# Kernel tuning notes

Measured on AMD Instinct MI355X. Metric: run time of the kernel, lower is better.

Reference implementation:

```python
import jax, jax.numpy as jnp
import numpy as np

B, C, N, K = 8, 192, 3136, 9
COUT = 384


def setup_inputs() -> dict:
    key = jax.random.key(0)
    k1, k2, k3, k4 = jax.random.split(key, 4)
    x = jax.random.normal(k1, (B, C, N, 1), dtype=jnp.float32)
    edge_index = jax.random.randint(k2, (2, B, N, K), 0, N, dtype=jnp.int64)
    # 1x1 conv params: BasicConv([2C, COUT]) with bias, act='relu'
    W = jax.random.normal(k3, (COUT, 2 * C), dtype=jnp.float32) * (1.0 / np.sqrt(2 * C))
    b = jax.random.normal(k4, (COUT,), dtype=jnp.float32) * 0.01
    return {"x": x, "edge_index": edge_index, "W": W, "b": b}


def _gather(xs, idx):
    # xs: [B, C, N]; idx: [B, N, K] -> [B, C, N, K]
    return jax.vmap(lambda xb, ib: xb[:, ib])(xs, idx)


def reference(x, edge_index, W, b):
    xs = x[..., 0]                       # [B, C, N]
    x_i = _gather(xs, edge_index[1])     # [B, C, N, K] center features
    x_j = _gather(xs, edge_index[0])     # [B, C, N, K] neighbor features
    feat = jnp.concatenate([x_i, x_j - x_i], axis=1)  # [B, 2C, N, K]
    # 1x1 conv + bias + relu
    h = jnp.einsum('oi,bink->bonk', W, feat) + b[None, :, None, None]
    h = jax.nn.relu(h)                   # [B, COUT, N, K]
    return jnp.max(h, axis=-1, keepdims=True)  # [B, COUT, N, 1]
```

## Files before the change

kernel.cpp:

```cpp
#include <hip/hip_runtime.h>
#include <hip/hip_bf16.h>


#define Bb   8
#define Cc   192
#define Nn   3136
#define Kk   9
#define CO   384
#define TWOC 384
#define JTOT 768
#define PADC 200

typedef short  short8 __attribute__((ext_vector_type(8)));
typedef float  f32x4  __attribute__((ext_vector_type(4)));

__device__ __forceinline__ float bf2f(unsigned int u16) {
    union { unsigned int i; float f; } c;
    c.i = u16 << 16;
    return c.f;
}
__device__ __forceinline__ short f2bf(float f) {
    __hip_bfloat16 h = __float2bfloat16(f);
    short s; __builtin_memcpy(&s, &h, 2); return s;
}

__global__ __launch_bounds__(64) void detect(const unsigned short* __restrict__ xu,
                                             const int* __restrict__ ei,
                                             int* __restrict__ flags) {
    const int lane = threadIdx.x;
    unsigned int u = xu[2 * lane];
    int bige = (((u >> 7) & 0xFFu) >= 0x88u);
    unsigned long long bf = __ballot(bige);
    int oddnz = (ei[2 * lane + 1] != 0);
    unsigned long long bo = __ballot(oddnz);
    if (lane == 0) {
        flags[0] = (bf != 0ull) ? 1 : 0;
        flags[1] = (bo == 0ull) ? 1 : 0;
    }
}

__global__ __launch_bounds__(256) void prep_AT(const void* __restrict__ W_,
                                               short* __restrict__ A_Tb,
                                               const int* __restrict__ flags) {
    const int fp32 = flags[0];
    int t = blockIdx.x * 256 + threadIdx.x;
    if (t >= JTOT * Cc) return;
    int j = t / Cc;
    int c = t - j * Cc;
    int row = (j < CO) ? j : (j - CO);
    float w1, w2;
    if (fp32) {
        const float* W = (const float*)W_;
        w1 = W[row * TWOC + c];  w2 = W[row * TWOC + Cc + c];
    } else {
        const unsigned short* W = (const unsigned short*)W_;
        w1 = bf2f(W[row * TWOC + c]);  w2 = bf2f(W[row * TWOC + Cc + c]);
    }
    A_Tb[(size_t)j * PADC + c] = f2bf((j < CO) ? (w1 - w2) : w2);
}

__global__ __launch_bounds__(256) void transpose_x(const void* __restrict__ x_,
                                                   short* __restrict__ xT,
                                                   const int* __restrict__ flags) {
    __shared__ float s[64][33];
    const int fp32 = flags[0];
    const int n0 = blockIdx.x * 64;
    const int c0 = blockIdx.y * 32;
    const int b  = blockIdx.z;
    const int t  = threadIdx.x;
    const int cl   = t >> 3;
    const int nseg = t & 7;

    if (fp32) {
        const float* p = (const float*)x_ + ((size_t)b * Cc + c0 + cl) * Nn + n0 + nseg * 8;
        float4 v0 = *(const float4*)p;
        float4 v1 = *(const float4*)(p + 4);
        int nb = nseg * 8;
        s[nb + 0][cl] = v0.x;  s[nb + 1][cl] = v0.y;
        s[nb + 2][cl] = v0.z;  s[nb + 3][cl] = v0.w;
        s[nb + 4][cl] = v1.x;  s[nb + 5][cl] = v1.y;
        s[nb + 6][cl] = v1.z;  s[nb + 7][cl] = v1.w;
    } else {
        const unsigned short* p = (const unsigned short*)x_ + ((size_t)b * Cc + c0 + cl) * Nn + n0 + nseg * 8;
        ushort4 u0 = *(const ushort4*)p;
        ushort4 u1 = *(const ushort4*)(p + 4);
        int nb = nseg * 8;
        s[nb + 0][cl] = bf2f(u0.x);  s[nb + 1][cl] = bf2f(u0.y);
        s[nb + 2][cl] = bf2f(u0.z);  s[nb + 3][cl] = bf2f(u0.w);
        s[nb + 4][cl] = bf2f(u1.x);  s[nb + 5][cl] = bf2f(u1.y);
        s[nb + 6][cl] = bf2f(u1.z);  s[nb + 7][cl] = bf2f(u1.w);
    }
    __syncthreads();

    const int nl = t >> 2;
    const int cs = t & 3;
    short8 o;
#pragma unroll
    for (int i = 0; i < 8; ++i) o[i] = f2bf(s[nl][cs * 8 + i]);
    *(short8*)(xT + ((size_t)b * Nn + n0 + nl) * PADC + c0 + cs * 8) = o;
}

#define MT 64
#define NT 256
#define KT 32
#define LPAD 40

__global__ __launch_bounds__(256) void gemm_mfma(const short* __restrict__ xT,
                                                 const short* __restrict__ A_Tb,
                                                 short* __restrict__ U,
                                                 short* __restrict__ V) {
    __shared__ short Asl[MT * LPAD];
    __shared__ short Bsl[NT * LPAD];

    const int n0 = blockIdx.x * MT;
    const int j0 = blockIdx.y * NT;
    const int b  = blockIdx.z;
    const int tid  = threadIdx.x;
    const int w    = tid >> 6;
    const int lane = tid & 63;
    const int col  = lane & 15;
    const int quad = lane >> 4;

    f32x4 acc[4][4];
#pragma unroll
    for (int i = 0; i < 4; ++i)
#pragma unroll
        for (int jf = 0; jf < 4; ++jf) acc[i][jf] = (f32x4)(0.0f);

    const int ar = tid >> 2;
    const int ag = tid & 3;

    for (int c0 = 0; c0 < Cc; c0 += KT) {
        *(short8*)(Asl + ar * LPAD + ag * 8) =
            *(const short8*)(xT + ((size_t)b * Nn + n0 + ar) * PADC + c0 + ag * 8);
#pragma unroll
        for (int h = 0; h < 4; ++h) {
            int row = h * 64 + ar;
            *(short8*)(Bsl + row * LPAD + ag * 8) =
                *(const short8*)(A_Tb + (size_t)(j0 + row) * PADC + c0 + ag * 8);
        }
        __syncthreads();

        short8 bf[4];
#pragma unroll
        for (int jf = 0; jf < 4; ++jf)
            bf[jf] = *(const short8*)(&Bsl[(w * 64 + jf * 16 + col) * LPAD + quad * 8]);
#pragma unroll
        for (int fm = 0; fm < 4; ++fm) {
            short8 a = *(const short8*)(&Asl[(fm * 16 + col) * LPAD + quad * 8]);
#pragma unroll
            for (int jf = 0; jf < 4; ++jf)
                acc[fm][jf] = __builtin_amdgcn_mfma_f32_16x16x32_bf16(a, bf[jf], acc[fm][jf], 0, 0, 0);
        }
        __syncthreads();
    }

    const int jbase = j0 + w * 64;
#pragma unroll
    for (int fn = 0; fn < 4; ++fn) {
        int j = jbase + fn * 16 + col;
        short* dst; int jj;
        if (j < CO) { dst = U; jj = j; } else { dst = V; jj = j - CO; }
#pragma unroll
        for (int fm = 0; fm < 4; ++fm) {
#pragma unroll
            for (int r = 0; r < 4; ++r) {
                int n = n0 + fm * 16 + quad * 4 + r;
                dst[((size_t)(b * Nn + n)) * CO + jj] = f2bf(acc[fm][fn][r]);
            }
        }
    }
}

__global__ __launch_bounds__(384) void gather_max(const int* __restrict__ ei,
                                                  const short* __restrict__ U,
                                                  const short* __restrict__ V,
                                                  const void* __restrict__ bias_,
                                                  void* __restrict__ out_,
                                                  const int* __restrict__ flags) {
    __shared__ float sm[32][193];
    __shared__ int si0[32][Kk];
    __shared__ int si1[32][Kk];

    const int fp32 = flags[0];
    const int is64 = flags[1];
    const int bid  = blockIdx.x;
    const int b    = bid & 7;
    const int rest = bid >> 3;
    const int half = rest / 98;
    const int n0   = (rest % 98) * 32;
    const int tid  = threadIdx.x;

    for (int s = tid; s < 32 * 2 * Kk; s += 384) {
        int ln = s / (2 * Kk);
        int slot = s - ln * (2 * Kk);
        int n = n0 + ln;
        size_t pos; int* dstp;
        if (slot < Kk) { pos = ((size_t)b * Nn + n) * Kk + slot;               dstp = &si0[ln][slot]; }
        else           { pos = ((size_t)(Bb + b) * Nn + n) * Kk + (slot - Kk); dstp = &si1[ln][slot - Kk]; }
        int v = is64 ? ei[2 * pos] : ei[pos];
        *dstp = (v < 0) ? 0 : (v >= Nn ? Nn - 1 : v);
    }
    __syncthreads();

    const int p   = tid % 96;
    const int seg = tid / 96;
    const int och = half * 192 + 2 * p;
    const unsigned short* Ub = (const unsigned short*)U + (size_t)b * Nn * CO;
    const unsigned short* Vb = (const unsigned short*)V + (size_t)b * Nn * CO;

    float b0, b1;
    if (fp32) {
        b0 = ((const float*)bias_)[och];
        b1 = ((const float*)bias_)[och + 1];
    } else {
        b0 = bf2f(((const unsigned short*)bias_)[och]);
        b1 = bf2f(((const unsigned short*)bias_)[och + 1]);
    }

    for (int ln = seg * 8; ln < seg * 8 + 8; ++ln) {
        float m0 = -INFINITY, m1 = -INFINITY;
#pragma unroll
        for (int k = 0; k < Kk; ++k) {
            unsigned int uu = *(const unsigned int*)(Ub + (size_t)si1[ln][k] * CO + och);
            unsigned int vv = *(const unsigned int*)(Vb + (size_t)si0[ln][k] * CO + och);
            m0 = fmaxf(m0, bf2f(uu & 0xffffu) + bf2f(vv & 0xffffu));
            m1 = fmaxf(m1, bf2f(uu >> 16) + bf2f(vv >> 16));
        }
        sm[ln][2 * p]     = fmaxf(m0 + b0, 0.0f);
        sm[ln][2 * p + 1] = fmaxf(m1 + b1, 0.0f);
    }
    __syncthreads();

    const int g = tid >> 5, l = tid & 31;
    if (fp32) {
        float* op = (float*)out_;
#pragma unroll
        for (int rr = 0; rr < 16; ++rr) {
            int ol = g * 16 + rr;
            int o  = half * 192 + ol;
            op[((size_t)b * CO + o) * Nn + n0 + l] = sm[l][ol];
        }
    } else {
        __hip_bfloat16* op = (__hip_bfloat16*)out_;
#pragma unroll
        for (int rr = 0; rr < 16; ++rr) {
            int ol = g * 16 + rr;
            int o  = half * 192 + ol;
            op[((size_t)b * CO + o) * Nn + n0 + l] = __float2bfloat16(sm[l][ol]);
        }
    }
}

extern "C" void kernel_launch(void* const* d_in, const int* in_sizes, int n_in,
                              void* d_out, int out_size, void* d_ws, size_t ws_size,
                              hipStream_t stream) {
    const void* x  = d_in[0];
    const int*  ei = (const int*)d_in[1];
    const void* W  = d_in[2];
    const void* bs = d_in[3];

    char* ws = (char*)d_ws;
    int*   flags = (int*)ws;
    short* A_Tb  = (short*)(ws + 1024);
    short* xT    = (short*)(ws + (512u << 10));
    short* U     = (short*)(ws + (16u << 20));
    short* V     = U + (size_t)Bb * Nn * CO;

    detect<<<1, 64, 0, stream>>>((const unsigned short*)x, ei, flags);

    prep_AT<<<(JTOT * Cc + 255) / 256, 256, 0, stream>>>(W, A_Tb, flags);

    dim3 gt(Nn / 64, Cc / 32, Bb);
    transpose_x<<<gt, 256, 0, stream>>>(x, xT, flags);

    dim3 g1(Nn / MT, JTOT / NT, Bb);
    gemm_mfma<<<g1, 256, 0, stream>>>(xT, A_Tb, U, V);

    gather_max<<<Bb * 2 * (Nn / 32), 384, 0, stream>>>(ei, U, V, bs, d_out, flags);
}
```

Before: 148.7 us.

## Fuse detect, weight prep and transpose into one kernel; interleave U/V output

Merges the type-detection, weight-difference prep and x transpose kernels into a single launch whose block ranges split the work. Each block re-derives the dtype flag locally, so it no longer waits on a separate detect kernel. The GEMM now writes U and V interleaved per node into one buffer with row stride 768 instead of two separate arrays, so the gather's U and V loads share a base pointer and sit closer together. This removes two kernel launches and their serial dependencies, at the cost of a small redundant ballot in every block.

```diff
diff --git a/kernel.cpp b/kernel.cpp
--- a/kernel.cpp
+++ b/kernel.cpp
@@ -24,80 +24,87 @@
     short s; __builtin_memcpy(&s, &h, 2); return s;
 }
 
-__global__ __launch_bounds__(64) void detect(const unsigned short* __restrict__ xu,
-                                             const int* __restrict__ ei,
-                                             int* __restrict__ flags) {
-    const int lane = threadIdx.x;
-    unsigned int u = xu[2 * lane];
-    int bige = (((u >> 7) & 0xFFu) >= 0x88u);
-    unsigned long long bf = __ballot(bige);
-    int oddnz = (ei[2 * lane + 1] != 0);
-    unsigned long long bo = __ballot(oddnz);
-    if (lane == 0) {
-        flags[0] = (bf != 0ull) ? 1 : 0;
-        flags[1] = (bo == 0ull) ? 1 : 0;
-    }
-}
-
-__global__ __launch_bounds__(256) void prep_AT(const void* __restrict__ W_,
-                                               short* __restrict__ A_Tb,
-                                               const int* __restrict__ flags) {
-    const int fp32 = flags[0];
-    int t = blockIdx.x * 256 + threadIdx.x;
-    if (t >= JTOT * Cc) return;
-    int j = t / Cc;
-    int c = t - j * Cc;
-    int row = (j < CO) ? j : (j - CO);
-    float w1, w2;
-    if (fp32) {
-        const float* W = (const float*)W_;
-        w1 = W[row * TWOC + c];  w2 = W[row * TWOC + Cc + c];
+__global__ __launch_bounds__(256) void prep_fused(const void* __restrict__ x_,
+                                                  const void* __restrict__ W_,
+                                                  const int* __restrict__ ei,
+                                                  short* __restrict__ xT,
+                                                  short* __restrict__ A_Tb,
+                                                  int* __restrict__ flags) {
+    __shared__ float s[64][33];
+    __shared__ int sflag;
+    const int tid = threadIdx.x;
+    const int bid = blockIdx.x;
+
+    if (tid < 64) {
+        unsigned int u = ((const unsigned short*)x_)[2 * tid];
+        int bige = (((u >> 7) & 0xFFu) >= 0x88u);
+        unsigned long long bf = __ballot(bige);
+        int f32 = (bf != 0ull) ? 1 : 0;
+        if (tid == 0) sflag = f32;
+        if (bid == 0) {
+            int oddnz = (ei[2 * tid + 1] != 0);
+            unsigned long long bo = __ballot(oddnz);
+            if (tid == 0) {
+                flags[0] = f32;
+                flags[1] = (bo == 0ull) ? 1 : 0;
+            }
+        }
+    }
+    __syncthreads();
+    const int fp32 = sflag;
+
+    if (bid < 2352) {
+        int b   = bid / 294;
+        int rem = bid - b * 294;
+        int ct  = rem / 49;
+        int nt  = rem - ct * 49;
+        const int n0 = nt * 64;
+        const int c0 = ct * 32;
+        const int cl   = tid >> 3;
+        const int nseg = tid & 7;
+
+        if (fp32) {
+            const float* p = (const float*)x_ + ((size_t)b * Cc + c0 + cl) * Nn + n0 + nseg * 8;
+            float4 v0 = *(const float4*)p;
+            float4 v1 = *(const float4*)(p + 4);
+            int nb = nseg * 8;
+            s[nb + 0][cl] = v0.x;  s[nb + 1][cl] = v0.y;
+            s[nb + 2][cl] = v0.z;  s[nb + 3][cl] = v0.w;
+            s[nb + 4][cl] = v1.x;  s[nb + 5][cl] = v1.y;
+            s[nb + 6][cl] = v1.z;  s[nb + 7][cl] = v1.w;
+        } else {
+            const unsigned short* p = (const unsigned short*)x_ + ((size_t)b * Cc + c0 + cl) * Nn + n0 + nseg * 8;
+            ushort4 u0 = *(const ushort4*)p;
+            ushort4 u1 = *(const ushort4*)(p + 4);
+            int nb = nseg * 8;
+            s[nb + 0][cl] = bf2f(u0.x);  s[nb + 1][cl] = bf2f(u0.y);
+            s[nb + 2][cl] = bf2f(u0.z);  s[nb + 3][cl] = bf2f(u0.w);
+            s[nb + 4][cl] = bf2f(u1.x);  s[nb + 5][cl] = bf2f(u1.y);
+            s[nb + 6][cl] = bf2f(u1.z);  s[nb + 7][cl] = bf2f(u1.w);
+        }
+        __syncthreads();
+
+        const int nl = tid >> 2;
+        const int cs = tid & 3;
+        short8 o;
+#pragma unroll
+        for (int i = 0; i < 8; ++i) o[i] = f2bf(s[nl][cs * 8 + i]);
+        *(short8*)(xT + ((size_t)b * Nn + n0 + nl) * PADC + c0 + cs * 8) = o;
     } else {
-        const unsigned short* W = (const unsigned short*)W_;
-        w1 = bf2f(W[row * TWOC + c]);  w2 = bf2f(W[row * TWOC + Cc + c]);
-    }
-    A_Tb[(size_t)j * PADC + c] = f2bf((j < CO) ? (w1 - w2) : w2);
-}
-
-__global__ __launch_bounds__(256) void transpose_x(const void* __restrict__ x_,
-                                                   short* __restrict__ xT,
-                                                   const int* __restrict__ flags) {
-    __shared__ float s[64][33];
-    const int fp32 = flags[0];
-    const int n0 = blockIdx.x * 64;
-    const int c0 = blockIdx.y * 32;
-    const int b  = blockIdx.z;
-    const int t  = threadIdx.x;
-    const int cl   = t >> 3;
-    const int nseg = t & 7;
-
-    if (fp32) {
-        const float* p = (const float*)x_ + ((size_t)b * Cc + c0 + cl) * Nn + n0 + nseg * 8;
-        float4 v0 = *(const float4*)p;
-        float4 v1 = *(const float4*)(p + 4);
-        int nb = nseg * 8;
-        s[nb + 0][cl] = v0.x;  s[nb + 1][cl] = v0.y;
-        s[nb + 2][cl] = v0.z;  s[nb + 3][cl] = v0.w;
-        s[nb + 4][cl] = v1.x;  s[nb + 5][cl] = v1.y;
-        s[nb + 6][cl] = v1.z;  s[nb + 7][cl] = v1.w;
-    } else {
-        const unsigned short* p = (const unsigned short*)x_ + ((size_t)b * Cc + c0 + cl) * Nn + n0 + nseg * 8;
-        ushort4 u0 = *(const ushort4*)p;
-        ushort4 u1 = *(const ushort4*)(p + 4);
-        int nb = nseg * 8;
-        s[nb + 0][cl] = bf2f(u0.x);  s[nb + 1][cl] = bf2f(u0.y);
-        s[nb + 2][cl] = bf2f(u0.z);  s[nb + 3][cl] = bf2f(u0.w);
-        s[nb + 4][cl] = bf2f(u1.x);  s[nb + 5][cl] = bf2f(u1.y);
-        s[nb + 6][cl] = bf2f(u1.z);  s[nb + 7][cl] = bf2f(u1.w);
-    }
-    __syncthreads();
-
-    const int nl = t >> 2;
-    const int cs = t & 3;
-    short8 o;
-#pragma unroll
-    for (int i = 0; i < 8; ++i) o[i] = f2bf(s[nl][cs * 8 + i]);
-    *(short8*)(xT + ((size_t)b * Nn + n0 + nl) * PADC + c0 + cs * 8) = o;
+        int t = (bid - 2352) * 256 + tid;
+        int j = t / Cc;
+        int c = t - j * Cc;
+        int row = (j < CO) ? j : (j - CO);
+        float w1, w2;
+        if (fp32) {
+            const float* W = (const float*)W_;
+            w1 = W[row * TWOC + c];  w2 = W[row * TWOC + Cc + c];
+        } else {
+            const unsigned short* W = (const unsigned short*)W_;
+            w1 = bf2f(W[row * TWOC + c]);  w2 = bf2f(W[row * TWOC + Cc + c]);
+        }
+        A_Tb[(size_t)j * PADC + c] = f2bf((j < CO) ? (w1 - w2) : w2);
+    }
 }
 
 #define MT 64
@@ -107,8 +114,7 @@
 
 __global__ __launch_bounds__(256) void gemm_mfma(const short* __restrict__ xT,
                                                  const short* __restrict__ A_Tb,
-                                                 short* __restrict__ U,
-                                                 short* __restrict__ V) {
+                                                 short* __restrict__ T) {
     __shared__ short Asl[MT * LPAD];
     __shared__ short Bsl[NT * LPAD];
 
@@ -159,22 +165,19 @@
 #pragma unroll
     for (int fn = 0; fn < 4; ++fn) {
         int j = jbase + fn * 16 + col;
-        short* dst; int jj;
-        if (j < CO) { dst = U; jj = j; } else { dst = V; jj = j - CO; }
 #pragma unroll
         for (int fm = 0; fm < 4; ++fm) {
 #pragma unroll
             for (int r = 0; r < 4; ++r) {
                 int n = n0 + fm * 16 + quad * 4 + r;
-                dst[((size_t)(b * Nn + n)) * CO + jj] = f2bf(acc[fm][fn][r]);
+                T[((size_t)(b * Nn + n)) * JTOT + j] = f2bf(acc[fm][fn][r]);
             }
         }
     }
 }
 
 __global__ __launch_bounds__(384) void gather_max(const int* __restrict__ ei,
-                                                  const short* __restrict__ U,
-                                                  const short* __restrict__ V,
+                                                  const short* __restrict__ T,
                                                   const void* __restrict__ bias_,
                                                   void* __restrict__ out_,
                                                   const int* __restrict__ flags) {
@@ -206,8 +209,7 @@
     const int p   = tid % 96;
     const int seg = tid / 96;
     const int och = half * 192 + 2 * p;
-    const unsigned short* Ub = (const unsigned short*)U + (size_t)b * Nn * CO;
-    const unsigned short* Vb = (const unsigned short*)V + (size_t)b * Nn * CO;
+    const unsigned short* Tb = (const unsigned short*)T + (size_t)b * Nn * JTOT;
 
     float b0, b1;
     if (fp32) {
@@ -222,8 +224,8 @@
         float m0 = -INFINITY, m1 = -INFINITY;
 #pragma unroll
         for (int k = 0; k < Kk; ++k) {
-            unsigned int uu = *(const unsigned int*)(Ub + (size_t)si1[ln][k] * CO + och);
-            unsigned int vv = *(const unsigned int*)(Vb + (size_t)si0[ln][k] * CO + och);
+            unsigned int uu = *(const unsigned int*)(Tb + (size_t)si1[ln][k] * JTOT + och);
+            unsigned int vv = *(const unsigned int*)(Tb + (size_t)si0[ln][k] * JTOT + CO + och);
             m0 = fmaxf(m0, bf2f(uu & 0xffffu) + bf2f(vv & 0xffffu));
             m1 = fmaxf(m1, bf2f(uu >> 16) + bf2f(vv >> 16));
         }
@@ -264,18 +266,12 @@
     int*   flags = (int*)ws;
     short* A_Tb  = (short*)(ws + 1024);
     short* xT    = (short*)(ws + (512u << 10));
-    short* U     = (short*)(ws + (16u << 20));
-    short* V     = U + (size_t)Bb * Nn * CO;
-
-    detect<<<1, 64, 0, stream>>>((const unsigned short*)x, ei, flags);
-
-    prep_AT<<<(JTOT * Cc + 255) / 256, 256, 0, stream>>>(W, A_Tb, flags);
-
-    dim3 gt(Nn / 64, Cc / 32, Bb);
-    transpose_x<<<gt, 256, 0, stream>>>(x, xT, flags);
+    short* T     = (short*)(ws + (11u << 20));
+
+    prep_fused<<<2352 + 576, 256, 0, stream>>>(x, W, ei, xT, A_Tb, flags);
 
     dim3 g1(Nn / MT, JTOT / NT, Bb);
-    gemm_mfma<<<g1, 256, 0, stream>>>(xT, A_Tb, U, V);
-
-    gather_max<<<Bb * 2 * (Nn / 32), 384, 0, stream>>>(ei, U, V, bs, d_out, flags);
-}
+    gemm_mfma<<<g1, 256, 0, stream>>>(xT, A_Tb, T);
+
+    gather_max<<<Bb * 2 * (Nn / 32), 384, 0, stream>>>(ei, T, bs, d_out, flags);
+}
```

Measured after the change: 146.2 us. No clear change (-1.6%).
